# Kernel tuning notes

Measured on AMD Instinct MI355X. Metric: run time of the kernel, lower is better.

The kernel has to match this reference:

```python
import jax, jax.numpy as jnp
import numpy as np

INF = 1000000.0
B, S, D, N, H = 2, 2048, 1024, 16, 64
T = 2 * S
NORM = 1.0 / np.sqrt(H)


def _rel_shift(x, k_len, shift=1):
    # x: [b, n, f, t] -> Transformer-XL relative shift -> [b, n, f, k_len]
    b, n, f, t = x.shape
    y = x.reshape(b, n, t, f)[:, :, shift:, :].reshape(b, n, f, t - shift)
    return y[:, :, :, :k_len]


def setup_inputs() -> dict:
    key = jax.random.key(0)
    ks = jax.random.split(key, 16)
    inp = {}
    inp['q'] = jax.random.normal(ks[0], (B, S, D), jnp.float32)
    inp['k'] = jax.random.normal(ks[1], (B, S, D), jnp.float32)
    inp['v'] = jax.random.normal(ks[2], (B, S, D), jnp.float32)
    inp['pos_enc'] = jax.random.normal(ks[3], (T, D), jnp.float32)
    seg_ids = jax.random.randint(ks[4], (B, S), 0, 2)
    inp['seg_mat'] = seg_ids[:, :, None] == seg_ids[:, None, :]  # [B,S,S] bool
    # causal mask: 1 where attention is forbidden (j > i)
    causal = (jnp.arange(S)[None, :] > jnp.arange(S)[:, None]).astype(jnp.float32)
    inp['attn_mask'] = jnp.broadcast_to(causal[None, None], (B, 1, S, S))
    std = np.sqrt(1.0 / (D + N * H))
    inp['qW'] = jax.random.normal(ks[5], (D, N, H), jnp.float32) * std
    inp['kW'] = jax.random.normal(ks[6], (D, N, H), jnp.float32) * std
    inp['kb'] = jnp.zeros((N, H), jnp.float32)
    inp['vW'] = jax.random.normal(ks[7], (D, N, H), jnp.float32) * std
    inp['vb'] = jnp.zeros((N, H), jnp.float32)
    inp['r_w_bias'] = jax.random.uniform(ks[8], (N, H), jnp.float32, 0.0, 0.1)
    inp['r_r_bias'] = jax.random.uniform(ks[9], (N, H), jnp.float32, 0.0, 0.1)
    inp['r_kernel'] = jax.random.uniform(ks[10], (D, N, H), jnp.float32, 0.0, 0.1)
    inp['r_s_bias'] = jax.random.uniform(ks[11], (N, H), jnp.float32, 0.0, 0.1)
    inp['seg_embed'] = jax.random.uniform(ks[12], (2, N, H), jnp.float32, 0.0, 0.1)
    inp['postW'] = jax.random.normal(ks[13], (N, H, D), jnp.float32) * std
    inp['postb'] = jnp.zeros((D,), jnp.float32)
    inp['ln_g'] = jnp.ones((D,), jnp.float32)
    inp['ln_b'] = jnp.zeros((D,), jnp.float32)
    return inp


def reference(q, k, v, pos_enc, seg_mat, attn_mask, qW, kW, kb, vW, vb,
              r_w_bias, r_r_bias, r_kernel, r_s_bias, seg_embed,
              postW, postb, ln_g, ln_b):
    # head projections
    q_head = jnp.einsum('bid,dnh->binh', q, qW) * NORM
    k_head = jnp.einsum('bjd,dnh->bjnh', k, kW) + kb
    v_head = jnp.einsum('bjd,dnh->bjnh', v, vW) + vb
    # content score (r_w_bias also scaled by normalizer)
    content = jnp.einsum('binh,bjnh->bnij', q_head + r_w_bias * NORM, k_head)
    # relative position bias (rel_shift branch, shift=1)
    q_r = q_head + r_r_bias * NORM
    r_head = jnp.einsum('td,dnh->tnh', pos_enc, r_kernel)
    bd = jnp.einsum('bfnh,tnh->bnft', q_r, r_head)  # [B,N,S,T]
    pos_bias = _rel_shift(bd, S, shift=1)           # [B,N,S,S]
    # segment bias
    sb = jnp.einsum('binh,snh->bnis', q_head + r_s_bias * NORM, seg_embed)
    diff, same = sb[..., 0:1], sb[..., 1:2]         # [B,N,S,1]
    seg_bias = jnp.where(seg_mat[:, None], same, diff)  # [B,N,S,S]
    # combine, mask, softmax
    score = content + pos_bias + seg_bias
    score = score.astype(jnp.float32) - INF * attn_mask
    dist = jax.nn.softmax(score, axis=-1)
    # attention output
    attn_vec = jnp.einsum('bnij,bjnh->binh', dist, v_head)
    attn_out = jnp.einsum('binh,nhd->bid', attn_vec, postW) + postb
    # residual + layer norm
    x = q + attn_out
    mu = jnp.mean(x, axis=-1, keepdims=True)
    var = jnp.var(x, axis=-1, keepdims=True)
    return (x - mu) * jax.lax.rsqrt(var + 1e-5) * ln_g + ln_b
```

## Files before the change

kernel.cpp:

```cpp
#include <hip/hip_runtime.h>
#include <hip/hip_bf16.h>

typedef __attribute__((ext_vector_type(8))) short bf16x8;
typedef __attribute__((ext_vector_type(4))) float f32x4;
typedef unsigned short ushort_t;

#define S_LEN 2048
#define DMODEL 1024
#define NORM_F 0.125f

__device__ __forceinline__ short f2b(float x) {
  union { float f; unsigned u; } c; c.f = x;
  unsigned r = (c.u + 0x7FFFu + ((c.u >> 16) & 1u)) >> 16;
  return (short)r;
}
__device__ __forceinline__ float b2f(ushort_t u) {
  union { unsigned u; float f; } c; c.u = ((unsigned)u) << 16; return c.f;
}
__device__ __forceinline__ unsigned cvtpk(float lo, float hi) {
  unsigned r;
  asm volatile("v_cvt_pk_bf16_f32 %0, %1, %2" : "=v"(r) : "v"(lo), "v"(hi));
  return r;
}
__device__ __forceinline__ uint4 pack8(float4 a, float4 b) {
  union { ushort_t us[8]; uint4 v; } o;
  o.us[0] = (ushort_t)f2b(a.x); o.us[1] = (ushort_t)f2b(a.y);
  o.us[2] = (ushort_t)f2b(a.z); o.us[3] = (ushort_t)f2b(a.w);
  o.us[4] = (ushort_t)f2b(b.x); o.us[5] = (ushort_t)f2b(b.y);
  o.us[6] = (ushort_t)f2b(b.z); o.us[7] = (ushort_t)f2b(b.w);
  return o.v;
}

__global__ void seg_extract_kernel(const unsigned int* __restrict__ seg_raw,
                                   unsigned* __restrict__ segw) {
  __shared__ int bad_int, bad_flt;
  int tid = threadIdx.x;
  if (tid == 0) { bad_int = 0; bad_flt = 0; }
  __syncthreads();
  for (int i = tid; i < 2048; i += 256) {
    unsigned v = seg_raw[i];
    if (v > 1u) atomicOr(&bad_int, 1);
    if (v != 0u && v != 0x3F800000u) atomicOr(&bad_flt, 1);
  }
  __syncthreads();
  int mode = bad_int ? (bad_flt ? 2 : 1) : 0;
  const unsigned char* u8 = (const unsigned char*)seg_raw;
  int P = blockIdx.x * 256 + tid;
  int b = P >> 11, i = P & 2047;
  size_t off = (size_t)b * S_LEN * S_LEN + i;
  int bit;
  if (mode == 0)      bit = (int)(seg_raw[off] & 1u);
  else if (mode == 1) bit = (seg_raw[off] != 0u) ? 1 : 0;
  else                bit = (int)(u8[off] & 1u);
  unsigned long long mk = __ballot(bit);
  if ((tid & 63) == 0) {
    segw[P >> 5] = (unsigned)mk;
    segw[(P >> 5) + 1] = (unsigned)(mk >> 32);
  }
}

__global__ __launch_bounds__(256) void convT_kernel(
    const float* __restrict__ s0, const float* __restrict__ s1,
    const float* __restrict__ s2, const float* __restrict__ s3,
    const float* __restrict__ s4,
    ushort_t* __restrict__ d0, ushort_t* __restrict__ d1,
    ushort_t* __restrict__ d2, ushort_t* __restrict__ d3,
    ushort_t* __restrict__ d4) {
  int z = blockIdx.z;
  const float* src = z == 0 ? s0 : z == 1 ? s1 : z == 2 ? s2 : z == 3 ? s3 : s4;
  ushort_t* dst = z == 0 ? d0 : z == 1 ? d1 : z == 2 ? d2 : z == 3 ? d3 : d4;
  __shared__ float Tl[64][68];
  int tid = threadIdx.x;
  int k0 = blockIdx.x * 64, n0 = blockIdx.y * 64;
#pragma unroll
  for (int it = 0; it < 4; ++it) {
    int idx = tid + it * 256;
    int r = idx >> 4, c4 = (idx & 15) * 4;
    *(float4*)&Tl[r][c4] = *(const float4*)(src + (size_t)(k0 + r) * 1024 + n0 + c4);
  }
  __syncthreads();
#pragma unroll
  for (int it = 0; it < 2; ++it) {
    int idx = tid + it * 256;
    int nn = idx >> 3, kc = idx & 7;
    union { ushort_t us[8]; uint4 v; } o;
#pragma unroll
    for (int e = 0; e < 8; ++e) o.us[e] = (ushort_t)f2b(Tl[kc * 8 + e][nn]);
    *(uint4*)(dst + (size_t)(n0 + nn) * 1024 + k0 + kc * 8) = o.v;
  }
}

__global__ __launch_bounds__(256) void gemm4_kernel(
    const float* __restrict__ a0, const float* __restrict__ a1,
    const float* __restrict__ a2, const float* __restrict__ a3,
    const ushort_t* __restrict__ w0, const ushort_t* __restrict__ w1,
    const ushort_t* __restrict__ w2, const ushort_t* __restrict__ w3,
    const float* __restrict__ kb, const float* __restrict__ vb,
    const float* __restrict__ rwb, const float* __restrict__ rrb,
    const float* __restrict__ rsb, const float* __restrict__ sem,
    ushort_t* __restrict__ qwb, ushort_t* __restrict__ qrb,
    float2* __restrict__ sbp,
    ushort_t* __restrict__ c1, ushort_t* __restrict__ c2,
    ushort_t* __restrict__ c3) {
  const int z = blockIdx.z;
  const float* A     = z == 0 ? a0 : z == 1 ? a1 : z == 2 ? a2 : a3;
  const ushort_t* Wt = z == 0 ? w0 : z == 1 ? w1 : z == 2 ? w2 : w3;

  __shared__ short A_lds[128][40];
  __shared__ short B_lds[128][40];
  const int tid = threadIdx.x;
  const int wave = tid >> 6, lane = tid & 63;
  const int r16 = lane & 15, g = lane >> 4;
  const int wm = wave >> 1, wn = wave & 1;
  const int m0 = blockIdx.x * 128, n0 = blockIdx.y * 128;
  const int sr = tid >> 2, sseg = (tid & 3) * 8;
  f32x4 acc[4][4] = {};
  float4 fa0a = *(const float4*)(A + (size_t)(m0 + sr) * 1024 + sseg);
  float4 fa0b = *(const float4*)(A + (size_t)(m0 + sr) * 1024 + sseg + 4);
  float4 fa1a = *(const float4*)(A + (size_t)(m0 + 64 + sr) * 1024 + sseg);
  float4 fa1b = *(const float4*)(A + (size_t)(m0 + 64 + sr) * 1024 + sseg + 4);
  uint4 rb0 = *(const uint4*)(Wt + (size_t)(n0 + sr) * 1024 + sseg);
  uint4 rb1 = *(const uint4*)(Wt + (size_t)(n0 + 64 + sr) * 1024 + sseg);
  for (int k0 = 0; k0 < 1024; k0 += 32) {
    *(uint4*)&A_lds[sr][sseg] = pack8(fa0a, fa0b);
    *(uint4*)&A_lds[64 + sr][sseg] = pack8(fa1a, fa1b);
    *(uint4*)&B_lds[sr][sseg] = rb0;
    *(uint4*)&B_lds[64 + sr][sseg] = rb1;
    __syncthreads();
    if (k0 + 32 < 1024) {
      fa0a = *(const float4*)(A + (size_t)(m0 + sr) * 1024 + k0 + 32 + sseg);
      fa0b = *(const float4*)(A + (size_t)(m0 + sr) * 1024 + k0 + 32 + sseg + 4);
      fa1a = *(const float4*)(A + (size_t)(m0 + 64 + sr) * 1024 + k0 + 32 + sseg);
      fa1b = *(const float4*)(A + (size_t)(m0 + 64 + sr) * 1024 + k0 + 32 + sseg + 4);
      rb0 = *(const uint4*)(Wt + (size_t)(n0 + sr) * 1024 + k0 + 32 + sseg);
      rb1 = *(const uint4*)(Wt + (size_t)(n0 + 64 + sr) * 1024 + k0 + 32 + sseg);
    }
    bf16x8 af[4], bfr[4];
#pragma unroll
    for (int fm = 0; fm < 4; ++fm)
      af[fm] = *(const bf16x8*)&A_lds[wm * 64 + fm * 16 + r16][g * 8];
#pragma unroll
    for (int fn = 0; fn < 4; ++fn)
      bfr[fn] = *(const bf16x8*)&B_lds[wn * 64 + fn * 16 + r16][g * 8];
#pragma unroll
    for (int fm = 0; fm < 4; ++fm)
#pragma unroll
      for (int fn = 0; fn < 4; ++fn)
        acc[fm][fn] = __builtin_amdgcn_mfma_f32_16x16x32_bf16(af[fm], bfr[fn], acc[fm][fn], 0, 0, 0);
    __syncthreads();
  }

  if (z == 0) {
    float rwbN[4], rrbN[4], rsbN[4], s0c[4], s1c[4];
#pragma unroll
    for (int fn = 0; fn < 4; ++fn) {
      int col = n0 + wn * 64 + fn * 16 + r16;
      rwbN[fn] = rwb[col] * NORM_F;
      rrbN[fn] = rrb[col] * NORM_F;
      rsbN[fn] = rsb[col] * NORM_F;
      s0c[fn] = sem[col];
      s1c[fn] = sem[1024 + col];
    }
    const int nI = (n0 >> 6) + wn;
#pragma unroll
    for (int fm = 0; fm < 4; ++fm)
#pragma unroll
      for (int rr = 0; rr < 4; ++rr) {
        int row = m0 + wm * 64 + fm * 16 + g * 4 + rr;
        float p0 = 0.f, p1 = 0.f;
#pragma unroll
        for (int fn = 0; fn < 4; ++fn) {
          float vv = acc[fm][fn][rr] * NORM_F;
          size_t off = (size_t)row * 1024 + n0 + wn * 64 + fn * 16 + r16;
          qwb[off] = (ushort_t)f2b(vv + rwbN[fn]);
          qrb[off] = (ushort_t)f2b(vv + rrbN[fn]);
          float qs = vv + rsbN[fn];
          p0 += qs * s0c[fn];
          p1 += qs * s1c[fn];
        }
        p0 += __shfl_xor(p0, 1); p0 += __shfl_xor(p0, 2);
        p0 += __shfl_xor(p0, 4); p0 += __shfl_xor(p0, 8);
        p1 += __shfl_xor(p1, 1); p1 += __shfl_xor(p1, 2);
        p1 += __shfl_xor(p1, 4); p1 += __shfl_xor(p1, 8);
        if (r16 == 0) {
          int bI = row >> 11, iI = row & 2047;
          sbp[((size_t)bI * 16 + nI) * 2048 + iI] = make_float2(p0, p1);
        }
      }
  } else {
    const float* bias = z == 1 ? kb : z == 2 ? vb : (const float*)nullptr;
    ushort_t* C = z == 1 ? c1 : z == 2 ? c2 : c3;
    float bv[4];
#pragma unroll
    for (int fn = 0; fn < 4; ++fn)
      bv[fn] = bias ? bias[n0 + wn * 64 + fn * 16 + r16] : 0.f;
#pragma unroll
    for (int fm = 0; fm < 4; ++fm)
#pragma unroll
      for (int fn = 0; fn < 4; ++fn)
#pragma unroll
        for (int rr = 0; rr < 4; ++rr) {
          float vv = acc[fm][fn][rr] + bv[fn];
          size_t off = (size_t)(m0 + wm * 64 + fm * 16 + g * 4 + rr) * 1024 +
                       n0 + wn * 64 + fn * 16 + r16;
          C[off] = (ushort_t)f2b(vv);
        }
  }
}

__global__ __launch_bounds__(256) void gemm_post_kernel(
    const ushort_t* __restrict__ A, const ushort_t* __restrict__ Wt,
    const float* __restrict__ bias, float* __restrict__ C) {
  __shared__ short A_lds[64][40];
  __shared__ short B_lds[128][40];
  const int tid = threadIdx.x;
  const int wave = tid >> 6, lane = tid & 63;
  const int r16 = lane & 15, g = lane >> 4;
  const int wm = wave >> 1, wn = wave & 1;
  const int m0 = blockIdx.x * 64, n0 = blockIdx.y * 128;
  const int sr = tid >> 2, sseg = (tid & 3) * 8;
  f32x4 acc[2][4] = {};
  uint4 ra0 = *(const uint4*)(A + (size_t)(m0 + sr) * 1024 + sseg);
  uint4 rb0 = *(const uint4*)(Wt + (size_t)(n0 + sr) * 1024 + sseg);
  uint4 rb1 = *(const uint4*)(Wt + (size_t)(n0 + 64 + sr) * 1024 + sseg);
  for (int k0 = 0; k0 < 1024; k0 += 32) {
    *(uint4*)&A_lds[sr][sseg] = ra0;
    *(uint4*)&B_lds[sr][sseg] = rb0;
    *(uint4*)&B_lds[64 + sr][sseg] = rb1;
    __syncthreads();
    if (k0 + 32 < 1024) {
      ra0 = *(const uint4*)(A + (size_t)(m0 + sr) * 1024 + k0 + 32 + sseg);
      rb0 = *(const uint4*)(Wt + (size_t)(n0 + sr) * 1024 + k0 + 32 + sseg);
      rb1 = *(const uint4*)(Wt + (size_t)(n0 + 64 + sr) * 1024 + k0 + 32 + sseg);
    }
    bf16x8 af[2], bfr[4];
#pragma unroll
    for (int fm = 0; fm < 2; ++fm)
      af[fm] = *(const bf16x8*)&A_lds[wm * 32 + fm * 16 + r16][g * 8];
#pragma unroll
    for (int fn = 0; fn < 4; ++fn)
      bfr[fn] = *(const bf16x8*)&B_lds[wn * 64 + fn * 16 + r16][g * 8];
#pragma unroll
    for (int fm = 0; fm < 2; ++fm)
#pragma unroll
      for (int fn = 0; fn < 4; ++fn)
        acc[fm][fn] = __builtin_amdgcn_mfma_f32_16x16x32_bf16(af[fm], bfr[fn], acc[fm][fn], 0, 0, 0);
    __syncthreads();
  }
  float bv[4];
#pragma unroll
  for (int fn = 0; fn < 4; ++fn)
    bv[fn] = bias ? bias[n0 + wn * 64 + fn * 16 + r16] : 0.f;
#pragma unroll
  for (int fm = 0; fm < 2; ++fm)
#pragma unroll
    for (int fn = 0; fn < 4; ++fn)
#pragma unroll
      for (int rr = 0; rr < 4; ++rr) {
        size_t off = (size_t)(m0 + wm * 32 + fm * 16 + g * 4 + rr) * 1024 +
                     n0 + wn * 64 + fn * 16 + r16;
        C[off] = acc[fm][fn][rr] + bv[fn];
      }
}

__global__ __launch_bounds__(256) void attn_kernel(
    const ushort_t* __restrict__ qwb, const ushort_t* __restrict__ qrb,
    const ushort_t* __restrict__ khb, const ushort_t* __restrict__ vhb,
    const ushort_t* __restrict__ rhb, const float2* __restrict__ sbp,
    const unsigned* __restrict__ segw, ushort_t* __restrict__ opart,
    float* __restrict__ ml) {
  __shared__ short Klds[64][64];
  __shared__ short Rlds[128][64];
  __shared__ short VsT[2][64][72];
  __shared__ short SP[4][1376];

  const int tid = threadIdx.x;
  const int w = tid >> 6, lane = tid & 63;
  const int r16 = lane & 15, g = lane >> 4;
  const int lin = (int)blockIdx.x;
  const int grp = (lin & 7) + ((lin >> 9) << 3);
  const int j = (lin >> 3) & 63;
  const int x = 31 - (j >> 1);
  const int hx = j & 1;
  const int i0 = x * 64;
  const int nh = (x + 2) >> 1;
  const int tbeg = hx ? nh : 0;
  const int tend = hx ? (x + 1) : nh;
  const int n = grp & 15, b = grp >> 4;
  const int BNS = 65536;
  const int rowbase = (b * 16 + n) * 2048 + i0;

  if (tbeg >= tend) {
    const int il0 = w * 16 + g * 4;
#pragma unroll
    for (int rr = 0; rr < 4; ++rr) {
#pragma unroll
      for (int s = 0; s < 4; ++s)
        opart[(size_t)(BNS + rowbase + il0 + rr) * 64 + s * 16 + r16] = 0;
      if (r16 == 0) {
        ml[2 * BNS + rowbase + il0 + rr] = -1e30f;
        ml[3 * BNS + rowbase + il0 + rr] = 0.f;
      }
    }
    return;
  }

  short* SPw = &SP[w][0];
  const int srow = tid >> 3, sg8 = (tid & 7) * 8;

  const int qrow = i0 + w * 16 + r16;
  const ushort_t* qwp = qwb + (size_t)(b * S_LEN + qrow) * DMODEL + n * 64 + g * 8;
  const ushort_t* qrp = qrb + (size_t)(b * S_LEN + qrow) * DMODEL + n * 64 + g * 8;
  bf16x8 qw[2], qr[2];
  qw[0] = *(const bf16x8*)qwp;  qw[1] = *(const bf16x8*)(qwp + 32);
  qr[0] = *(const bf16x8*)qrp;  qr[1] = *(const bf16x8*)(qrp + 32);
  float2 sbv = sbp[((size_t)b * 16 + n) * 2048 + qrow];
  const float sb0 = sbv.x, sb1 = sbv.y;
  const int ai = (segw[b * 64 + (qrow >> 5)] >> (qrow & 31)) & 1;
  const int iw0 = i0 + w * 16;

  {
    const int j0 = tbeg * 64;
    const int W0 = 2048 + j0 - i0 - 63;
#pragma unroll
    for (int it = 0; it < 2; ++it) {
      int qk = tid + it * 256, row = qk >> 3, cl = qk & 7;
      uint4 kv = *(const uint4*)(khb + (size_t)(b * S_LEN + j0 + row) * DMODEL + n * 64 + cl * 8);
      *(uint4*)&Klds[row][(cl ^ (row & 7)) * 8] = kv;
    }
#pragma unroll
    for (int it = 0; it < 4; ++it) {
      int qk = tid + it * 256, row = qk >> 3, cl = qk & 7;
      uint4 rv = *(const uint4*)(rhb + (size_t)(W0 + row) * DMODEL + n * 64 + cl * 8);
      *(uint4*)&Rlds[row][(cl ^ (row & 7)) * 8] = rv;
    }
#pragma unroll
    for (int it = 0; it < 2; ++it) {
      int jj = srow + it * 32;
      union { uint4 v; ushort_t us[8]; } vv;
      vv.v = *(const uint4*)(vhb + (size_t)(b * S_LEN + j0 + jj) * DMODEL + n * 64 + sg8);
#pragma unroll
      for (int e = 0; e < 8; ++e) {
        int hh = sg8 + e;
        VsT[0][hh][((jj >> 3) ^ (hh >> 3)) * 8 + (jj & 7)] = (short)vv.us[e];
      }
    }
  }

  float m_r = -1e30f, l_r = 0.f;
  f32x4 o[4] = {};

  for (int t = tbeg; t < tend; ++t) {
    const int j0 = t * 64;
    const int tt = (t - tbeg) & 1;
    const bool hasn = (t + 1 < tend);
    __syncthreads();

    uint4 kpf[2], rpf[4], vpf[2];
    if (hasn) {
      const int j0n = j0 + 64;
      const int W0n = 2048 + j0n - i0 - 63;
#pragma unroll
      for (int it = 0; it < 2; ++it) {
        int qk = tid + it * 256, row = qk >> 3, cl = qk & 7;
        kpf[it] = *(const uint4*)(khb + (size_t)(b * S_LEN + j0n + row) * DMODEL + n * 64 + cl * 8);
      }
#pragma unroll
      for (int it = 0; it < 4; ++it) {
        int qk = tid + it * 256, row = qk >> 3, cl = qk & 7;
        rpf[it] = *(const uint4*)(rhb + (size_t)(W0n + row) * DMODEL + n * 64 + cl * 8);
      }
#pragma unroll
      for (int it = 0; it < 2; ++it)
        vpf[it] = *(const uint4*)(vhb + (size_t)(b * S_LEN + j0n + srow + it * 32) * DMODEL + n * 64 + sg8);
    }
    unsigned wlo = segw[b * 64 + (j0 >> 5)];
    unsigned whi = segw[b * 64 + (j0 >> 5) + 1];

    __builtin_amdgcn_s_setprio(1);
    f32x4 cf[4] = {};
#pragma unroll
    for (int s = 0; s < 4; ++s) {
      int row = s * 16 + r16;
      bf16x8 k0 = *(const bf16x8*)&Klds[row][(g ^ (row & 7)) * 8];
      bf16x8 k1 = *(const bf16x8*)&Klds[row][((4 + g) ^ (row & 7)) * 8];
      cf[s] = __builtin_amdgcn_mfma_f32_16x16x32_bf16(k0, qw[0], cf[s], 0, 0, 0);
      cf[s] = __builtin_amdgcn_mfma_f32_16x16x32_bf16(k1, qw[1], cf[s], 0, 0, 0);
    }
#pragma unroll
    for (int sp = 0; sp < 5; ++sp) {
      int row = 48 - w * 16 + sp * 16 + r16;
      bf16x8 r0 = *(const bf16x8*)&Rlds[row][(g ^ (row & 7)) * 8];
      bf16x8 r1 = *(const bf16x8*)&Rlds[row][((4 + g) ^ (row & 7)) * 8];
      f32x4 pf = {};
      pf = __builtin_amdgcn_mfma_f32_16x16x32_bf16(r0, qr[0], pf, 0, 0, 0);
      pf = __builtin_amdgcn_mfma_f32_16x16x32_bf16(r1, qr[1], pf, 0, 0, 0);
      uint2 pw;
      pw.x = cvtpk(pf[0], pf[1]);
      pw.y = cvtpk(pf[2], pf[3]);
      *(uint2*)&SPw[r16 * 84 + sp * 16 + g * 4] = pw;
    }
    __builtin_amdgcn_s_setprio(0);
    ushort_t pu[4][4];
#pragma unroll
    for (int s = 0; s < 4; ++s)
#pragma unroll
      for (int rr = 0; rr < 4; ++rr)
        pu[s][rr] = (ushort_t)SPw[r16 * 84 + (15 - r16) + s * 16 + g * 4 + rr];
    float vals[4][4];
    float vmax = -1e30f;
    const bool diag = (t == x);
#pragma unroll
    for (int s = 0; s < 4; ++s) {
      unsigned word = (s < 2) ? wlo : whi;
#pragma unroll
      for (int rr = 0; rr < 4; ++rr) {
        int p = s * 16 + g * 4 + rr;
        int bitv = (word >> (p & 31)) & 1;
        float sv = cf[s][rr] + b2f(pu[s][rr]) + ((bitv == ai) ? sb1 : sb0);
        if (diag && (p > w * 16 + r16)) sv -= 1e6f;
        vals[s][rr] = sv;
        vmax = fmaxf(vmax, sv);
      }
    }
    vmax = fmaxf(vmax, __shfl_xor(vmax, 16));
    vmax = fmaxf(vmax, __shfl_xor(vmax, 32));
    float scl = 1.f;
    bool resc = !__all(vmax <= m_r + 8.f);
    if (resc) {
      float mnew = fmaxf(m_r, vmax);
      scl = __expf(m_r - mnew);
      m_r = mnew;
    }
    float pex[4][4];
    float psum = 0.f;
#pragma unroll
    for (int s = 0; s < 4; ++s)
#pragma unroll
      for (int rr = 0; rr < 4; ++rr) {
        pex[s][rr] = __expf(vals[s][rr] - m_r);
        psum += pex[s][rr];
      }
    l_r = l_r * scl + psum;
#pragma unroll
    for (int s = 0; s < 4; ++s) {
      uint2 pw;
      pw.x = cvtpk(pex[s][0], pex[s][1]);
      pw.y = cvtpk(pex[s][2], pex[s][3]);
      *(uint2*)&SPw[r16 * 72 + s * 16 + g * 4] = pw;
    }
    __syncthreads();

    if (hasn) {
#pragma unroll
      for (int it = 0; it < 2; ++it) {
        int qk = tid + it * 256, row = qk >> 3, cl = qk & 7;
        *(uint4*)&Klds[row][(cl ^ (row & 7)) * 8] = kpf[it];
      }
#pragma unroll
      for (int it = 0; it < 4; ++it) {
        int qk = tid + it * 256, row = qk >> 3, cl = qk & 7;
        *(uint4*)&Rlds[row][(cl ^ (row & 7)) * 8] = rpf[it];
      }
      const int dst = tt ^ 1;
#pragma unroll
      for (int it = 0; it < 2; ++it) {
        int jj = srow + it * 32;
        union { uint4 v; ushort_t us[8]; } vv; vv.v = vpf[it];
#pragma unroll
        for (int e = 0; e < 8; ++e) {
          int hh = sg8 + e;
          VsT[dst][hh][((jj >> 3) ^ (hh >> 3)) * 8 + (jj & 7)] = (short)vv.us[e];
        }
      }
    }
    if (resc) {
      float sclb[4];
#pragma unroll
      for (int rr = 0; rr < 4; ++rr) sclb[rr] = __shfl(scl, g * 4 + rr);
#pragma unroll
      for (int s = 0; s < 4; ++s)
#pragma unroll
        for (int rr = 0; rr < 4; ++rr) o[s][rr] *= sclb[rr];
    }
    bf16x8 pa0 = *(const bf16x8*)&SPw[r16 * 72 + g * 8];
    bf16x8 pa1 = *(const bf16x8*)&SPw[r16 * 72 + 32 + g * 8];
    __builtin_amdgcn_s_setprio(1);
#pragma unroll
    for (int s = 0; s < 4; ++s) {
      int hh = s * 16 + r16;
      bf16x8 v0 = *(const bf16x8*)&VsT[tt][hh][(g ^ (hh >> 3)) * 8];
      bf16x8 v1 = *(const bf16x8*)&VsT[tt][hh][((4 + g) ^ (hh >> 3)) * 8];
      o[s] = __builtin_amdgcn_mfma_f32_16x16x32_bf16(pa0, v0, o[s], 0, 0, 0);
      o[s] = __builtin_amdgcn_mfma_f32_16x16x32_bf16(pa1, v1, o[s], 0, 0, 0);
    }
    __builtin_amdgcn_s_setprio(0);
  }

  float l_row = l_r;
  l_row += __shfl_xor(l_row, 16);
  l_row += __shfl_xor(l_row, 32);
  if (lane < 16) {
    ml[hx * 2 * BNS + rowbase + w * 16 + r16] = m_r;
    ml[(hx * 2 + 1) * BNS + rowbase + w * 16 + r16] = l_row;
  }
#pragma unroll
  for (int s = 0; s < 4; ++s)
#pragma unroll
    for (int rr = 0; rr < 4; ++rr) {
      const int il = w * 16 + g * 4 + rr;
      opart[(size_t)(hx * BNS + rowbase + il) * 64 + s * 16 + r16] = (ushort_t)f2b(o[s][rr]);
    }
}

__global__ __launch_bounds__(256) void merge_kernel(
    const ushort_t* __restrict__ opart, const float* __restrict__ ml,
    ushort_t* __restrict__ av) {
  const int BNS = 65536;
  int row = blockIdx.x * 4 + (threadIdx.x >> 6);
  int lane = threadIdx.x & 63;
  float m0 = ml[row], l0 = ml[BNS + row];
  float m1 = ml[2 * BNS + row], l1 = ml[3 * BNS + row];
  float m = fmaxf(m0, m1);
  float a0 = __expf(m0 - m), a1 = __expf(m1 - m);
  float inv = 1.f / (l0 * a0 + l1 * a1);
  float o0 = b2f(opart[(size_t)row * 64 + lane]);
  float o1 = b2f(opart[(size_t)(BNS + row) * 64 + lane]);
  float ov = (o0 * a0 + o1 * a1) * inv;
  int bI = row >> 15, nI = (row >> 11) & 15, iI = row & 2047;
  av[(size_t)(bI * 2048 + iI) * 1024 + nI * 64 + lane] = (ushort_t)f2b(ov);
}

__global__ __launch_bounds__(256) void ln_kernel(
    const float* __restrict__ q, const float* __restrict__ ao,
    const float* __restrict__ ln_g, const float* __restrict__ ln_b,
    float* __restrict__ out) {
  int row = blockIdx.x;
  const float* xq = q + (size_t)row * 1024;
  const float* xa = ao + (size_t)row * 1024;
  float x[4], lsum = 0.f, lsq = 0.f;
#pragma unroll
  for (int e = 0; e < 4; ++e) {
    int d = threadIdx.x + e * 256;
    x[e] = xq[d] + xa[d];
    lsum += x[e]; lsq += x[e] * x[e];
  }
  for (int off = 1; off < 64; off <<= 1) {
    lsum += __shfl_xor(lsum, off);
    lsq += __shfl_xor(lsq, off);
  }
  __shared__ float red[8];
  int wv = threadIdx.x >> 6, ln = threadIdx.x & 63;
  if (ln == 0) { red[wv] = lsum; red[4 + wv] = lsq; }
  __syncthreads();
  lsum = red[0] + red[1] + red[2] + red[3];
  lsq = red[4] + red[5] + red[6] + red[7];
  float mu = lsum * (1.f / 1024.f);
  float var = lsq * (1.f / 1024.f) - mu * mu;
  float inv = rsqrtf(var + 1e-5f);
#pragma unroll
  for (int e = 0; e < 4; ++e) {
    int d = threadIdx.x + e * 256;
    out[(size_t)row * 1024 + d] = (x[e] - mu) * inv * ln_g[d] + ln_b[d];
  }
}

extern "C" void kernel_launch(void* const* d_in, const int* in_sizes, int n_in,
                              void* d_out, int out_size, void* d_ws, size_t ws_size,
                              hipStream_t stream) {
  const float* q   = (const float*)d_in[0];
  const float* k   = (const float*)d_in[1];
  const float* v   = (const float*)d_in[2];
  const float* pe  = (const float*)d_in[3];
  const void*  seg = d_in[4];
  const float* qW  = (const float*)d_in[6];
  const float* kW  = (const float*)d_in[7];
  const float* kb  = (const float*)d_in[8];
  const float* vW  = (const float*)d_in[9];
  const float* vb  = (const float*)d_in[10];
  const float* rwb = (const float*)d_in[11];
  const float* rrb = (const float*)d_in[12];
  const float* rK  = (const float*)d_in[13];
  const float* rsb = (const float*)d_in[14];
  const float* sem = (const float*)d_in[15];
  const float* pW  = (const float*)d_in[16];
  const float* pb  = (const float*)d_in[17];
  const float* lng = (const float*)d_in[18];
  const float* lnb = (const float*)d_in[19];
  float* out = (float*)d_out;

  const size_t MB = 1u << 20;
  char* W = (char*)d_ws;
  ushort_t* qwb  = (ushort_t*)(W + 0 * MB);
  ushort_t* qrb  = (ushort_t*)(W + 8 * MB);
  ushort_t* opart = (ushort_t*)(W + 16 * MB);
  ushort_t* wtq  = (ushort_t*)(W + 32 * MB);
  ushort_t* wtk  = (ushort_t*)(W + 34 * MB);
  ushort_t* wtv  = (ushort_t*)(W + 36 * MB);
  ushort_t* wtr  = (ushort_t*)(W + 38 * MB);
  ushort_t* wtp  = (ushort_t*)(W + 40 * MB);
  ushort_t* av   = (ushort_t*)(W + 42 * MB);
  ushort_t* kh   = (ushort_t*)(W + 50 * MB);
  ushort_t* vh   = (ushort_t*)(W + 58 * MB);
  ushort_t* rh   = (ushort_t*)(W + 66 * MB);
  unsigned* segw = (unsigned*)(W + 74 * MB);
  float2*   sbp  = (float2*)(W + 74 * MB + 65536);
  float*    ml   = (float*)(W + 75 * MB);
  float*    ao   = (float*)(W + 50 * MB);

  seg_extract_kernel<<<dim3(16), dim3(256), 0, stream>>>((const unsigned int*)seg, segw);
  convT_kernel<<<dim3(16, 16, 5), dim3(256), 0, stream>>>(qW, kW, vW, rK, pW,
                                                          wtq, wtk, wtv, wtr, wtp);
  gemm4_kernel<<<dim3(32, 8, 4), dim3(256), 0, stream>>>(
      q, k, v, pe, wtq, wtk, wtv, wtr, kb, vb, rwb, rrb, rsb, sem,
      qwb, qrb, sbp, kh, vh, rh);

  attn_kernel<<<dim3(2048), dim3(256), 0, stream>>>(qwb, qrb, kh, vh, rh,
                                                    sbp, segw, opart, ml);
  merge_kernel<<<dim3(16384), dim3(256), 0, stream>>>(opart, ml, av);

  gemm_post_kernel<<<dim3(64, 8), dim3(256), 0, stream>>>(av, wtp, pb, ao);
  ln_kernel<<<dim3(4096), dim3(256), 0, stream>>>(q, ao, lng, lnb, out);
}
```

Measured before the change: 252.4 us.

## Fuse split-softmax merge into post-projection GEMM A-load and shrink attention LDS padding

Removes the separate merge kernel. The output-projection GEMM now reads the two partial attention outputs and their max/sum statistics directly, combining and normalizing them while building each A tile. This avoids writing and re-reading the intermediate attention vector and saves one kernel launch. The cost is that the rescale factors are recomputed for every N-block and K-step, so the ml loads and exp calls are repeated. The attention kernel's VsT and SP shared-memory padding is also reduced, which lowers LDS use per block and may allow more resident blocks per CU, at the risk of more bank conflicts.

```diff
diff --git a/kernel.cpp b/kernel.cpp
--- a/kernel.cpp
+++ b/kernel.cpp
@@ -209,8 +209,10 @@
 }
 
 __global__ __launch_bounds__(256) void gemm_post_kernel(
-    const ushort_t* __restrict__ A, const ushort_t* __restrict__ Wt,
-    const float* __restrict__ bias, float* __restrict__ C) {
+    const ushort_t* __restrict__ op, const float* __restrict__ ml,
+    const ushort_t* __restrict__ Wt, const float* __restrict__ bias,
+    float* __restrict__ C) {
+  const int BNS = 65536;
   __shared__ short A_lds[64][40];
   __shared__ short B_lds[128][40];
   const int tid = threadIdx.x;
@@ -219,8 +221,30 @@
   const int wm = wave >> 1, wn = wave & 1;
   const int m0 = blockIdx.x * 64, n0 = blockIdx.y * 128;
   const int sr = tid >> 2, sseg = (tid & 3) * 8;
+  const int arow = m0 + sr;
+  const int bI = arow >> 11, iI = arow & 2047;
+
+  auto loadA = [&](int kcol) -> uint4 {
+    size_t rowI = ((size_t)bI * 16 + (kcol >> 6)) * 2048 + iI;
+    float m0v = ml[rowI], l0 = ml[BNS + rowI];
+    float m1v = ml[2 * BNS + rowI], l1 = ml[3 * BNS + rowI];
+    float m = fmaxf(m0v, m1v);
+    float a0 = __expf(m0v - m), a1 = __expf(m1v - m);
+    float inv = 1.f / (l0 * a0 + l1 * a1);
+    a0 *= inv; a1 *= inv;
+    int hc = kcol & 63;
+    union { uint4 v; ushort_t us[8]; } u0, u1;
+    u0.v = *(const uint4*)(op + rowI * 64 + hc);
+    u1.v = *(const uint4*)(op + ((size_t)BNS + rowI) * 64 + hc);
+    union { ushort_t us[8]; uint4 v; } o;
+#pragma unroll
+    for (int e = 0; e < 8; ++e)
+      o.us[e] = (ushort_t)f2b(b2f(u0.us[e]) * a0 + b2f(u1.us[e]) * a1);
+    return o.v;
+  };
+
   f32x4 acc[2][4] = {};
-  uint4 ra0 = *(const uint4*)(A + (size_t)(m0 + sr) * 1024 + sseg);
+  uint4 ra0 = loadA(sseg);
   uint4 rb0 = *(const uint4*)(Wt + (size_t)(n0 + sr) * 1024 + sseg);
   uint4 rb1 = *(const uint4*)(Wt + (size_t)(n0 + 64 + sr) * 1024 + sseg);
   for (int k0 = 0; k0 < 1024; k0 += 32) {
@@ -229,7 +253,7 @@
     *(uint4*)&B_lds[64 + sr][sseg] = rb1;
     __syncthreads();
     if (k0 + 32 < 1024) {
-      ra0 = *(const uint4*)(A + (size_t)(m0 + sr) * 1024 + k0 + 32 + sseg);
+      ra0 = loadA(k0 + 32 + sseg);
       rb0 = *(const uint4*)(Wt + (size_t)(n0 + sr) * 1024 + k0 + 32 + sseg);
       rb1 = *(const uint4*)(Wt + (size_t)(n0 + 64 + sr) * 1024 + k0 + 32 + sseg);
     }
@@ -271,8 +295,8 @@
     float* __restrict__ ml) {
   __shared__ short Klds[64][64];
   __shared__ short Rlds[128][64];
-  __shared__ short VsT[2][64][72];
-  __shared__ short SP[4][1376];
+  __shared__ short VsT[2][64][64];
+  __shared__ short SP[4][1344];
 
   const int tid = threadIdx.x;
   const int w = tid >> 6, lane = tid & 63;
@@ -511,24 +535,6 @@
       const int il = w * 16 + g * 4 + rr;
       opart[(size_t)(hx * BNS + rowbase + il) * 64 + s * 16 + r16] = (ushort_t)f2b(o[s][rr]);
     }
-}
-
-__global__ __launch_bounds__(256) void merge_kernel(
-    const ushort_t* __restrict__ opart, const float* __restrict__ ml,
-    ushort_t* __restrict__ av) {
-  const int BNS = 65536;
-  int row = blockIdx.x * 4 + (threadIdx.x >> 6);
-  int lane = threadIdx.x & 63;
-  float m0 = ml[row], l0 = ml[BNS + row];
-  float m1 = ml[2 * BNS + row], l1 = ml[3 * BNS + row];
-  float m = fmaxf(m0, m1);
-  float a0 = __expf(m0 - m), a1 = __expf(m1 - m);
-  float inv = 1.f / (l0 * a0 + l1 * a1);
-  float o0 = b2f(opart[(size_t)row * 64 + lane]);
-  float o1 = b2f(opart[(size_t)(BNS + row) * 64 + lane]);
-  float ov = (o0 * a0 + o1 * a1) * inv;
-  int bI = row >> 15, nI = (row >> 11) & 15, iI = row & 2047;
-  av[(size_t)(bI * 2048 + iI) * 1024 + nI * 64 + lane] = (ushort_t)f2b(ov);
 }
 
 __global__ __launch_bounds__(256) void ln_kernel(
@@ -599,7 +605,6 @@
   ushort_t* wtv  = (ushort_t*)(W + 36 * MB);
   ushort_t* wtr  = (ushort_t*)(W + 38 * MB);
   ushort_t* wtp  = (ushort_t*)(W + 40 * MB);
-  ushort_t* av   = (ushort_t*)(W + 42 * MB);
   ushort_t* kh   = (ushort_t*)(W + 50 * MB);
   ushort_t* vh   = (ushort_t*)(W + 58 * MB);
   ushort_t* rh   = (ushort_t*)(W + 66 * MB);
@@ -617,8 +622,7 @@
 
   attn_kernel<<<dim3(2048), dim3(256), 0, stream>>>(qwb, qrb, kh, vh, rh,
                                                     sbp, segw, opart, ml);
-  merge_kernel<<<dim3(16384), dim3(256), 0, stream>>>(opart, ml, av);
-
-  gemm_post_kernel<<<dim3(64, 8), dim3(256), 0, stream>>>(av, wtp, pb, ao);
+
+  gemm_post_kernel<<<dim3(64, 8), dim3(256), 0, stream>>>(opart, ml, wtp, pb, ao);
   ln_kernel<<<dim3(4096), dim3(256), 0, stream>>>(q, ao, lng, lnb, out);
 }
```

Measured after the change: 259.7 us. 2.9% more time.
